# Optimization experiments

Measured on AMD Instinct MI355X. Metric: run time of the kernel, lower is better.

The kernel has to match this reference:

```python
import jax, jax.numpy as jnp
import numpy as np

N = 100_000   # nodes
E = 1_600_000 # edges (avg degree 16)
IN_DIM = 128
OUT_DIM = 64
NEG_SLOPE = 0.2  # PyG GATConv default


def setup_inputs() -> dict:
    key = jax.random.key(0)
    k_x, k_ei, k_w, k_as, k_ad = jax.random.split(key, 5)
    x = jax.random.normal(k_x, (N, IN_DIM), dtype=jnp.float32)
    edge_index = jax.random.randint(k_ei, (2, E), 0, N, dtype=jnp.int32)
    # GATConv params (heads=1): linear weight, attention vectors, output bias
    W = jax.random.normal(k_w, (IN_DIM, OUT_DIM), dtype=jnp.float32) / np.sqrt(IN_DIM)
    a_src = jax.random.normal(k_as, (OUT_DIM,), dtype=jnp.float32) * 0.1
    a_dst = jax.random.normal(k_ad, (OUT_DIM,), dtype=jnp.float32) * 0.1
    bias = jnp.zeros((OUT_DIM,), dtype=jnp.float32)
    return {"x": x, "edge_index": edge_index, "W": W, "a_src": a_src, "a_dst": a_dst, "bias": bias}


def reference(x, edge_index, W, a_src, a_dst, bias):
    # PyG GATConv, heads=1, add_self_loops=True
    h = x @ W                                   # [N, OUT]
    loop = jnp.arange(N, dtype=edge_index.dtype)
    ei = jnp.concatenate([edge_index, jnp.stack([loop, loop])], axis=1)  # [2, E+N]
    src, dst = ei[0], ei[1]
    # per-node attention logits, gathered per edge
    alpha_s = h @ a_src                         # [N]
    alpha_d = h @ a_dst                         # [N]
    e = alpha_s[src] + alpha_d[dst]             # [E+N]
    e = jnp.where(e > 0, e, NEG_SLOPE * e)      # leaky_relu
    # segment softmax over edges sharing the same destination node
    m = jax.ops.segment_max(e, dst, num_segments=N)   # every node has a self loop
    ex = jnp.exp(e - m[dst])
    s = jax.ops.segment_sum(ex, dst, num_segments=N)
    alpha = ex / s[dst]                         # [E+N]
    # weighted scatter-add of source messages
    out = jax.ops.segment_sum(alpha[:, None] * h[src], dst, num_segments=N)  # [N, OUT]
    return out + bias
```

## Files before the change

### kernel.cpp

```cpp
#include <hip/hip_runtime.h>
#include <hip/hip_bf16.h>

#ifndef NEG_SLOPE
#define NEG_SLOPE 0.2f
#endif

#define GRP_SHIFT 9
#define GRP_SIZE 512
#define NGMAX 256
#define MS_CHUNK 8192
#define BKT_CAP 10240

typedef short bf16x8 __attribute__((ext_vector_type(8)));
typedef float f32x4 __attribute__((ext_vector_type(4)));

__device__ __forceinline__ unsigned short f2bf(float f) {
    union { float f; unsigned int u; } c; c.f = f;
    unsigned int r = (c.u + 0x7FFFu + ((c.u >> 16) & 1u)) >> 16;
    return (unsigned short)r;
}
__device__ __forceinline__ float bf2f(unsigned short u) {
    union { unsigned int u; float f; } c; c.u = ((unsigned int)u) << 16;
    return c.f;
}
__device__ __forceinline__ float bflo(unsigned int u) {
    union { unsigned int u; float f; } c; c.u = u << 16;
    return c.f;
}
__device__ __forceinline__ float bfhi(unsigned int u) {
    union { unsigned int u; float f; } c; c.u = u & 0xffff0000u;
    return c.f;
}

__global__ __launch_bounds__(256) void gemm_kernel(
    const float* __restrict__ x, const float* __restrict__ W,
    const float* __restrict__ a_src, const float* __restrict__ a_dst,
    unsigned short* __restrict__ hb, float* __restrict__ as_,
    float* __restrict__ ad_, int* __restrict__ cursor, int N, int NG)
{
    __shared__ unsigned short xb[64 * 136];
    __shared__ unsigned short wt[64 * 136];

    const int tid = threadIdx.x;
    const int r0 = blockIdx.x * 64;

    if (blockIdx.x == 0) {
        for (int i = tid; i < NG; i += 256) cursor[i] = i * BKT_CAP;
    }

    for (int idx = tid; idx < 2048; idx += 256) {
        const int r = idx >> 5;
        const int c4 = idx & 31;
        const int row = r0 + r;
        float4 v = make_float4(0.f, 0.f, 0.f, 0.f);
        if (row < N) v = ((const float4*)(x + (size_t)row * 128))[c4];
        ushort4 o;
        o.x = f2bf(v.x); o.y = f2bf(v.y); o.z = f2bf(v.z); o.w = f2bf(v.w);
        *(ushort4*)(xb + r * 136 + c4 * 4) = o;
    }
    {
        const int n = tid & 63;
        const int kb = (tid >> 6) * 32;
        for (int kk = 0; kk < 32; ++kk) {
            const int k = kb + kk;
            wt[n * 136 + k] = f2bf(W[k * 64 + n]);
        }
    }
    __syncthreads();

    const int wv = tid >> 6;
    const int lane = tid & 63;
    const int m16 = lane & 15;
    const int quad = lane >> 4;

    f32x4 acc[4];
#pragma unroll
    for (int ct = 0; ct < 4; ++ct) acc[ct] = (f32x4){0.f, 0.f, 0.f, 0.f};

    const unsigned short* xrow = xb + (wv * 16 + m16) * 136;
#pragma unroll
    for (int kq = 0; kq < 4; ++kq) {
        const int k0 = kq * 32;
        const bf16x8 a = *(const bf16x8*)(xrow + k0 + quad * 8);
#pragma unroll
        for (int ct = 0; ct < 4; ++ct) {
            const bf16x8 b = *(const bf16x8*)(wt + (ct * 16 + m16) * 136 + k0 + quad * 8);
            acc[ct] = __builtin_amdgcn_mfma_f32_16x16x32_bf16(a, b, acc[ct], 0, 0, 0);
        }
    }

#pragma unroll
    for (int ct = 0; ct < 4; ++ct) {
#pragma unroll
        for (int rg = 0; rg < 4; ++rg) {
            const int row = r0 + wv * 16 + quad * 4 + rg;
            if (row < N) hb[(size_t)row * 64 + ct * 16 + m16] = f2bf(acc[ct][rg]);
        }
    }

    float asv[4], adv[4];
#pragma unroll
    for (int ct = 0; ct < 4; ++ct) {
        asv[ct] = a_src[ct * 16 + m16];
        adv[ct] = a_dst[ct * 16 + m16];
    }
#pragma unroll
    for (int rg = 0; rg < 4; ++rg) {
        float ps = acc[0][rg] * asv[0] + acc[1][rg] * asv[1] +
                   acc[2][rg] * asv[2] + acc[3][rg] * asv[3];
        float pd = acc[0][rg] * adv[0] + acc[1][rg] * adv[1] +
                   acc[2][rg] * adv[2] + acc[3][rg] * adv[3];
#pragma unroll
        for (int off = 1; off < 16; off <<= 1) {
            ps += __shfl_xor(ps, off);
            pd += __shfl_xor(pd, off);
        }
        const int row = r0 + wv * 16 + quad * 4 + rg;
        if (m16 == 0 && row < N) { as_[row] = ps; ad_[row] = pd; }
    }
}

__global__ __launch_bounds__(256) void multisplit_kernel(
    const int* __restrict__ ei, int* __restrict__ cursor,
    unsigned int* __restrict__ pairs, int E, int NG)
{
    __shared__ unsigned int ls_pack[MS_CHUNK];
    __shared__ unsigned char ls_g[MS_CHUNK];
    __shared__ int ls_hist[NGMAX];
    __shared__ int ls_gb[NGMAX];
    __shared__ int ls_wsum[4];

    const int tid = threadIdx.x;
    const int cs = blockIdx.x * MS_CHUNK;
    const int n = min(MS_CHUNK, E - cs);
    const int* srcp = ei + cs;
    const int* dstp = ei + E + cs;

    ls_hist[tid] = 0;
    __syncthreads();
    for (int i = tid; i < n; i += 256)
        atomicAdd(&ls_hist[dstp[i] >> GRP_SHIFT], 1);
    __syncthreads();

    const int h = ls_hist[tid];
    const int lane = tid & 63;
    int incl = h;
#pragma unroll
    for (int off = 1; off < 64; off <<= 1) {
        const int t = __shfl_up(incl, off);
        if (lane >= off) incl += t;
    }
    const int wv = tid >> 6;
    if (lane == 63) ls_wsum[wv] = incl;
    __syncthreads();
    int wpre = 0;
    for (int w = 0; w < wv; ++w) wpre += ls_wsum[w];
    const int excl = wpre + incl - h;
    if (tid < NG && h > 0) {
        const int gb = atomicAdd(&cursor[tid], h);
        ls_gb[tid] = gb - excl;
    }
    __syncthreads();
    ls_hist[tid] = excl;
    __syncthreads();

    for (int i = tid; i < n; i += 256) {
        const int src = srcp[i];
        const int dst = dstp[i];
        const int g = dst >> GRP_SHIFT;
        const int idx = atomicAdd(&ls_hist[g], 1);
        ls_pack[idx] = ((unsigned int)src << GRP_SHIFT) | (unsigned int)(dst & (GRP_SIZE - 1));
        ls_g[idx] = (unsigned char)g;
    }
    __syncthreads();

    for (int i = tid; i < n; i += 256) {
        const int g = ls_g[i];
        const int pos = ls_gb[g] + i;
        if (pos < (g + 1) * BKT_CAP)
            pairs[pos] = ls_pack[i];
    }
}

__global__ __launch_bounds__(256) void group_sort_kernel(
    const unsigned int* __restrict__ pairs, const int* __restrict__ cursor,
    unsigned int* __restrict__ meta, int* __restrict__ csr, int N)
{
    __shared__ int sdeg[GRP_SIZE];
    __shared__ int scur[GRP_SIZE];
    __shared__ int swsum[4];
    __shared__ int ssrc[BKT_CAP];
    const int g = blockIdx.x;
    const int tid = threadIdx.x;
    const int eb0 = g * BKT_CAP;
    const int cnt = min(cursor[g] - eb0, BKT_CAP);

    sdeg[tid] = 0;
    sdeg[tid + 256] = 0;
    __syncthreads();
    for (int i = tid; i < cnt; i += 256)
        atomicAdd(&sdeg[pairs[eb0 + i] & (GRP_SIZE - 1)], 1);
    __syncthreads();

    const int b0 = tid * 2;
    const int h0 = sdeg[b0], h1 = sdeg[b0 + 1];
    const int s = h0 + h1;
    const int lane = tid & 63;
    int incl = s;
#pragma unroll
    for (int off = 1; off < 64; off <<= 1) {
        const int t = __shfl_up(incl, off);
        if (lane >= off) incl += t;
    }
    const int wv = tid >> 6;
    if (lane == 63) swsum[wv] = incl;
    __syncthreads();
    int wpre = 0;
    for (int w = 0; w < wv; ++w) wpre += swsum[w];
    const int excl = wpre + incl - s;
    scur[b0] = excl;
    scur[b0 + 1] = excl + h0;
    {
        const int n0 = (g << GRP_SHIFT) + b0;
        if (n0 < N)
            meta[n0] = ((unsigned int)(eb0 + excl) << 10) | (unsigned int)min(h0, 1023);
        if (n0 + 1 < N)
            meta[n0 + 1] = ((unsigned int)(eb0 + excl + h0) << 10) | (unsigned int)min(h1, 1023);
    }
    __syncthreads();

    for (int i = tid; i < cnt; i += 256) {
        const unsigned int p = pairs[eb0 + i];
        const int idx = atomicAdd(&scur[p & (GRP_SIZE - 1)], 1);
        ssrc[idx] = (int)(p >> GRP_SHIFT);
    }
    __syncthreads();
    for (int i = tid; i < cnt; i += 256)
        csr[eb0 + i] = ssrc[i];
}

__global__ __launch_bounds__(256) void aggregate_kernel(
    const unsigned short* __restrict__ h, const float* __restrict__ as_,
    const float* __restrict__ ad_, const unsigned int* __restrict__ meta,
    const int* __restrict__ csr, const float* __restrict__ bias,
    float* __restrict__ out, int N)
{
    const int wid = (blockIdx.x * 256 + threadIdx.x) >> 6;
    const int lane = threadIdx.x & 63;
    if (wid >= N) return;

    const unsigned int mt = meta[wid];
    const int p0 = (int)(mt >> 10);
    const int deg = (int)(mt & 1023u);
    const float adi = ad_[wid];
    float e0 = as_[wid] + adi;
    e0 = e0 > 0.f ? e0 : NEG_SLOPE * e0;

    if (deg <= 63) {
        int s = wid;
        float e = -1e30f;
        if (lane < deg) {
            s = csr[p0 + lane];
            const float t = as_[s] + adi;
            e = t > 0.f ? t : NEG_SLOPE * t;
        } else if (lane == deg) {
            e = e0;
        }
        float m = e;
#pragma unroll
        for (int off = 1; off < 64; off <<= 1) m = fmaxf(m, __shfl_xor(m, off));
        const float pe = __expf(e - m);
        float l = pe;
#pragma unroll
        for (int off = 1; off < 64; off <<= 1) l += __shfl_xor(l, off);

        const int half = lane >> 5;
        const int l5 = lane & 31;
        const unsigned int* hb32 = (const unsigned int*)h;
        float acc0 = 0.f, acc1 = 0.f;
        const int npair = (deg + 2) >> 1;

        int jp = 0;
        for (; jp + 4 <= npair; jp += 4) {
            const int sl0 = (jp    ) * 2 + half;
            const int sl1 = (jp + 1) * 2 + half;
            const int sl2 = (jp + 2) * 2 + half;
            const int sl3 = (jp + 3) * 2 + half;
            const int s0 = __shfl(s, sl0), s1 = __shfl(s, sl1);
            const int s2 = __shfl(s, sl2), s3 = __shfl(s, sl3);
            const float w0 = __shfl(pe, sl0), w1 = __shfl(pe, sl1);
            const float w2 = __shfl(pe, sl2), w3 = __shfl(pe, sl3);
            const unsigned int u0 = hb32[s0 * 32 + l5];
            const unsigned int u1 = hb32[s1 * 32 + l5];
            const unsigned int u2 = hb32[s2 * 32 + l5];
            const unsigned int u3 = hb32[s3 * 32 + l5];
            acc0 += w0 * bflo(u0); acc1 += w0 * bfhi(u0);
            acc0 += w1 * bflo(u1); acc1 += w1 * bfhi(u1);
            acc0 += w2 * bflo(u2); acc1 += w2 * bfhi(u2);
            acc0 += w3 * bflo(u3); acc1 += w3 * bfhi(u3);
        }
        for (; jp < npair; ++jp) {
            const int sl = jp * 2 + half;
            const int sj = __shfl(s, sl);
            const float wj = __shfl(pe, sl);
            const unsigned int u = hb32[sj * 32 + l5];
            acc0 += wj * bflo(u);
            acc1 += wj * bfhi(u);
        }
        acc0 += __shfl_xor(acc0, 32);
        acc1 += __shfl_xor(acc1, 32);
        if (half == 0) {
            const float2 bv = ((const float2*)bias)[l5];
            float2 o;
            o.x = acc0 / l + bv.x;
            o.y = acc1 / l + bv.y;
            ((float2*)(out + (size_t)wid * 64))[l5] = o;
        }
    } else {
        float m = e0, ll = 1.f;
        float acc = bf2f(h[(size_t)wid * 64 + lane]);
        const int p1 = p0 + deg;
        for (int p = p0; p < p1; ++p) {
            const int sj = csr[p];
            float ee = as_[sj] + adi;
            ee = ee > 0.f ? ee : NEG_SLOPE * ee;
            const float nm = fmaxf(m, ee);
            const float sc = __expf(m - nm);
            const float pp = __expf(ee - nm);
            ll = ll * sc + pp;
            acc = acc * sc + pp * bf2f(h[(size_t)sj * 64 + lane]);
            m = nm;
        }
        out[(size_t)wid * 64 + lane] = acc / ll + bias[lane];
    }
}

extern "C" void kernel_launch(void* const* d_in, const int* in_sizes, int n_in,
                              void* d_out, int out_size, void* d_ws, size_t ws_size,
                              hipStream_t stream)
{
    const float* x     = (const float*)d_in[0];
    const int*   ei    = (const int*)d_in[1];
    const float* W     = (const float*)d_in[2];
    const float* a_src = (const float*)d_in[3];
    const float* a_dst = (const float*)d_in[4];
    const float* bias  = (const float*)d_in[5];
    float* out = (float*)d_out;

    const int N = in_sizes[0] / 128;
    const int E = in_sizes[1] / 2;
    const int NG = (N + GRP_SIZE - 1) >> GRP_SHIFT;
    const int nchunk = (E + MS_CHUNK - 1) / MS_CHUNK;

    unsigned short* hb = (unsigned short*)d_ws;
    float* alpha_s = (float*)(hb + (size_t)N * 64);
    float* alpha_d = alpha_s + N;
    int* cursor = (int*)(alpha_d + N);
    unsigned int* meta = (unsigned int*)(cursor + NG);
    int* csr = (int*)(meta + N);
    unsigned int* pairs = (unsigned int*)(csr + (size_t)NG * BKT_CAP);

    gemm_kernel<<<(N + 63) / 64, 256, 0, stream>>>(x, W, a_src, a_dst, hb,
                                                   alpha_s, alpha_d, cursor, N, NG);
    multisplit_kernel<<<nchunk, 256, 0, stream>>>(ei, cursor, pairs, E, NG);
    group_sort_kernel<<<NG, 256, 0, stream>>>(pairs, cursor, meta, csr, N);
    aggregate_kernel<<<(N + 3) / 4, 256, 0, stream>>>(hb, alpha_s, alpha_d, meta,
                                                      csr, bias, out, N);
}
```

Baseline: 215.0 us.

## Fuse GEMM with edge multisplit, widen group sort, process two nodes per wave

The GEMM and the edge multisplit now run as one launch with branch-selected block roles and a shared-memory union, and the cursor is zeroed by a memset so the two independent stages can overlap. The group sort runs with 1024 threads per block, one thread per destination slot. Aggregation assigns two destination nodes to each wave and interleaves their gathers to raise memory-level parallelism. In exchange, the fused kernel's shared-memory footprint follows the larger multisplit layout, and the paired loop does wasted shuffles and gathers when the two degrees differ.

```diff
diff --git a/kernel.cpp b/kernel.cpp
--- a/kernel.cpp
+++ b/kernel.cpp
@@ -32,211 +32,246 @@
     return c.f;
 }
 
-__global__ __launch_bounds__(256) void gemm_kernel(
+struct GemmSmem {
+    unsigned short xb[64 * 136];
+    unsigned short wt[64 * 136];
+};
+struct MsSmem {
+    unsigned int pack[MS_CHUNK];
+    unsigned char gtag[MS_CHUNK];
+    int hist[NGMAX];
+    int gb[NGMAX];
+    int wsum[4];
+};
+union FusedSmem {
+    GemmSmem g;
+    MsSmem m;
+};
+
+__global__ __launch_bounds__(256) void gemm_ms_kernel(
     const float* __restrict__ x, const float* __restrict__ W,
     const float* __restrict__ a_src, const float* __restrict__ a_dst,
     unsigned short* __restrict__ hb, float* __restrict__ as_,
-    float* __restrict__ ad_, int* __restrict__ cursor, int N, int NG)
+    float* __restrict__ ad_, const int* __restrict__ ei,
+    int* __restrict__ cursor, unsigned int* __restrict__ pairs,
+    int N, int E, int NG, int gemmBlocks)
 {
-    __shared__ unsigned short xb[64 * 136];
-    __shared__ unsigned short wt[64 * 136];
-
+    __shared__ FusedSmem sm;
     const int tid = threadIdx.x;
-    const int r0 = blockIdx.x * 64;
-
-    if (blockIdx.x == 0) {
-        for (int i = tid; i < NG; i += 256) cursor[i] = i * BKT_CAP;
-    }
-
-    for (int idx = tid; idx < 2048; idx += 256) {
-        const int r = idx >> 5;
-        const int c4 = idx & 31;
-        const int row = r0 + r;
-        float4 v = make_float4(0.f, 0.f, 0.f, 0.f);
-        if (row < N) v = ((const float4*)(x + (size_t)row * 128))[c4];
-        ushort4 o;
-        o.x = f2bf(v.x); o.y = f2bf(v.y); o.z = f2bf(v.z); o.w = f2bf(v.w);
-        *(ushort4*)(xb + r * 136 + c4 * 4) = o;
-    }
-    {
-        const int n = tid & 63;
-        const int kb = (tid >> 6) * 32;
-        for (int kk = 0; kk < 32; ++kk) {
-            const int k = kb + kk;
-            wt[n * 136 + k] = f2bf(W[k * 64 + n]);
-        }
-    }
-    __syncthreads();
-
-    const int wv = tid >> 6;
-    const int lane = tid & 63;
-    const int m16 = lane & 15;
-    const int quad = lane >> 4;
-
-    f32x4 acc[4];
-#pragma unroll
-    for (int ct = 0; ct < 4; ++ct) acc[ct] = (f32x4){0.f, 0.f, 0.f, 0.f};
-
-    const unsigned short* xrow = xb + (wv * 16 + m16) * 136;
-#pragma unroll
-    for (int kq = 0; kq < 4; ++kq) {
-        const int k0 = kq * 32;
-        const bf16x8 a = *(const bf16x8*)(xrow + k0 + quad * 8);
+
+    if ((int)blockIdx.x < gemmBlocks) {
+        unsigned short* xb = sm.g.xb;
+        unsigned short* wt = sm.g.wt;
+        const int r0 = blockIdx.x * 64;
+
+        for (int idx = tid; idx < 2048; idx += 256) {
+            const int r = idx >> 5;
+            const int c4 = idx & 31;
+            const int row = r0 + r;
+            float4 v = make_float4(0.f, 0.f, 0.f, 0.f);
+            if (row < N) v = ((const float4*)(x + (size_t)row * 128))[c4];
+            ushort4 o;
+            o.x = f2bf(v.x); o.y = f2bf(v.y); o.z = f2bf(v.z); o.w = f2bf(v.w);
+            *(ushort4*)(xb + r * 136 + c4 * 4) = o;
+        }
+        {
+            const int n = tid & 63;
+            const int kb = (tid >> 6) * 32;
+            for (int kk = 0; kk < 32; ++kk) {
+                const int k = kb + kk;
+                wt[n * 136 + k] = f2bf(W[k * 64 + n]);
+            }
+        }
+        __syncthreads();
+
+        const int wv = tid >> 6;
+        const int lane = tid & 63;
+        const int m16 = lane & 15;
+        const int quad = lane >> 4;
+
+        f32x4 acc[4];
+#pragma unroll
+        for (int ct = 0; ct < 4; ++ct) acc[ct] = (f32x4){0.f, 0.f, 0.f, 0.f};
+
+        const unsigned short* xrow = xb + (wv * 16 + m16) * 136;
+#pragma unroll
+        for (int kq = 0; kq < 4; ++kq) {
+            const int k0 = kq * 32;
+            const bf16x8 a = *(const bf16x8*)(xrow + k0 + quad * 8);
+#pragma unroll
+            for (int ct = 0; ct < 4; ++ct) {
+                const bf16x8 b = *(const bf16x8*)(wt + (ct * 16 + m16) * 136 + k0 + quad * 8);
+                acc[ct] = __builtin_amdgcn_mfma_f32_16x16x32_bf16(a, b, acc[ct], 0, 0, 0);
+            }
+        }
+
 #pragma unroll
         for (int ct = 0; ct < 4; ++ct) {
-            const bf16x8 b = *(const bf16x8*)(wt + (ct * 16 + m16) * 136 + k0 + quad * 8);
-            acc[ct] = __builtin_amdgcn_mfma_f32_16x16x32_bf16(a, b, acc[ct], 0, 0, 0);
-        }
-    }
-
-#pragma unroll
-    for (int ct = 0; ct < 4; ++ct) {
+#pragma unroll
+            for (int rg = 0; rg < 4; ++rg) {
+                const int row = r0 + wv * 16 + quad * 4 + rg;
+                if (row < N) hb[(size_t)row * 64 + ct * 16 + m16] = f2bf(acc[ct][rg]);
+            }
+        }
+
+        float asv[4], adv[4];
+#pragma unroll
+        for (int ct = 0; ct < 4; ++ct) {
+            asv[ct] = a_src[ct * 16 + m16];
+            adv[ct] = a_dst[ct * 16 + m16];
+        }
 #pragma unroll
         for (int rg = 0; rg < 4; ++rg) {
+            float ps = acc[0][rg] * asv[0] + acc[1][rg] * asv[1] +
+                       acc[2][rg] * asv[2] + acc[3][rg] * asv[3];
+            float pd = acc[0][rg] * adv[0] + acc[1][rg] * adv[1] +
+                       acc[2][rg] * adv[2] + acc[3][rg] * adv[3];
+#pragma unroll
+            for (int off = 1; off < 16; off <<= 1) {
+                ps += __shfl_xor(ps, off);
+                pd += __shfl_xor(pd, off);
+            }
             const int row = r0 + wv * 16 + quad * 4 + rg;
-            if (row < N) hb[(size_t)row * 64 + ct * 16 + m16] = f2bf(acc[ct][rg]);
-        }
-    }
-
-    float asv[4], adv[4];
-#pragma unroll
-    for (int ct = 0; ct < 4; ++ct) {
-        asv[ct] = a_src[ct * 16 + m16];
-        adv[ct] = a_dst[ct * 16 + m16];
-    }
-#pragma unroll
-    for (int rg = 0; rg < 4; ++rg) {
-        float ps = acc[0][rg] * asv[0] + acc[1][rg] * asv[1] +
-                   acc[2][rg] * asv[2] + acc[3][rg] * asv[3];
-        float pd = acc[0][rg] * adv[0] + acc[1][rg] * adv[1] +
-                   acc[2][rg] * adv[2] + acc[3][rg] * adv[3];
-#pragma unroll
-        for (int off = 1; off < 16; off <<= 1) {
-            ps += __shfl_xor(ps, off);
-            pd += __shfl_xor(pd, off);
-        }
-        const int row = r0 + wv * 16 + quad * 4 + rg;
-        if (m16 == 0 && row < N) { as_[row] = ps; ad_[row] = pd; }
-    }
-}
-
-__global__ __launch_bounds__(256) void multisplit_kernel(
-    const int* __restrict__ ei, int* __restrict__ cursor,
-    unsigned int* __restrict__ pairs, int E, int NG)
-{
-    __shared__ unsigned int ls_pack[MS_CHUNK];
-    __shared__ unsigned char ls_g[MS_CHUNK];
-    __shared__ int ls_hist[NGMAX];
-    __shared__ int ls_gb[NGMAX];
-    __shared__ int ls_wsum[4];
-
-    const int tid = threadIdx.x;
-    const int cs = blockIdx.x * MS_CHUNK;
-    const int n = min(MS_CHUNK, E - cs);
-    const int* srcp = ei + cs;
-    const int* dstp = ei + E + cs;
-
-    ls_hist[tid] = 0;
-    __syncthreads();
-    for (int i = tid; i < n; i += 256)
-        atomicAdd(&ls_hist[dstp[i] >> GRP_SHIFT], 1);
-    __syncthreads();
-
-    const int h = ls_hist[tid];
-    const int lane = tid & 63;
-    int incl = h;
-#pragma unroll
-    for (int off = 1; off < 64; off <<= 1) {
-        const int t = __shfl_up(incl, off);
-        if (lane >= off) incl += t;
-    }
-    const int wv = tid >> 6;
-    if (lane == 63) ls_wsum[wv] = incl;
-    __syncthreads();
-    int wpre = 0;
-    for (int w = 0; w < wv; ++w) wpre += ls_wsum[w];
-    const int excl = wpre + incl - h;
-    if (tid < NG && h > 0) {
-        const int gb = atomicAdd(&cursor[tid], h);
-        ls_gb[tid] = gb - excl;
-    }
-    __syncthreads();
-    ls_hist[tid] = excl;
-    __syncthreads();
-
-    for (int i = tid; i < n; i += 256) {
-        const int src = srcp[i];
-        const int dst = dstp[i];
-        const int g = dst >> GRP_SHIFT;
-        const int idx = atomicAdd(&ls_hist[g], 1);
-        ls_pack[idx] = ((unsigned int)src << GRP_SHIFT) | (unsigned int)(dst & (GRP_SIZE - 1));
-        ls_g[idx] = (unsigned char)g;
-    }
-    __syncthreads();
-
-    for (int i = tid; i < n; i += 256) {
-        const int g = ls_g[i];
-        const int pos = ls_gb[g] + i;
-        if (pos < (g + 1) * BKT_CAP)
-            pairs[pos] = ls_pack[i];
-    }
-}
-
-__global__ __launch_bounds__(256) void group_sort_kernel(
+            if (m16 == 0 && row < N) { as_[row] = ps; ad_[row] = pd; }
+        }
+    } else {
+        unsigned int* ls_pack = sm.m.pack;
+        unsigned char* ls_g = sm.m.gtag;
+        int* ls_hist = sm.m.hist;
+        int* ls_gb = sm.m.gb;
+        int* ls_wsum = sm.m.wsum;
+
+        const int cid = (int)blockIdx.x - gemmBlocks;
+        const int cs = cid * MS_CHUNK;
+        const int n = min(MS_CHUNK, E - cs);
+        const int* srcp = ei + cs;
+        const int* dstp = ei + E + cs;
+
+        ls_hist[tid] = 0;
+        __syncthreads();
+        for (int i = tid; i < n; i += 256)
+            atomicAdd(&ls_hist[dstp[i] >> GRP_SHIFT], 1);
+        __syncthreads();
+
+        const int h = ls_hist[tid];
+        const int lane = tid & 63;
+        int incl = h;
+#pragma unroll
+        for (int off = 1; off < 64; off <<= 1) {
+            const int t = __shfl_up(incl, off);
+            if (lane >= off) incl += t;
+        }
+        const int wv = tid >> 6;
+        if (lane == 63) ls_wsum[wv] = incl;
+        __syncthreads();
+        int wpre = 0;
+        for (int w = 0; w < wv; ++w) wpre += ls_wsum[w];
+        const int excl = wpre + incl - h;
+        if (tid < NG && h > 0) {
+            const int old = atomicAdd(&cursor[tid], h);
+            ls_gb[tid] = tid * BKT_CAP + old - excl;
+        }
+        __syncthreads();
+        ls_hist[tid] = excl;
+        __syncthreads();
+
+        for (int i = tid; i < n; i += 256) {
+            const int src = srcp[i];
+            const int dst = dstp[i];
+            const int g = dst >> GRP_SHIFT;
+            const int idx = atomicAdd(&ls_hist[g], 1);
+            ls_pack[idx] = ((unsigned int)src << GRP_SHIFT) | (unsigned int)(dst & (GRP_SIZE - 1));
+            ls_g[idx] = (unsigned char)g;
+        }
+        __syncthreads();
+
+        for (int i = tid; i < n; i += 256) {
+            const int g = ls_g[i];
+            const int pos = ls_gb[g] + i;
+            if (pos < (g + 1) * BKT_CAP)
+                pairs[pos] = ls_pack[i];
+        }
+    }
+}
+
+__global__ __launch_bounds__(1024) void group_sort_kernel(
     const unsigned int* __restrict__ pairs, const int* __restrict__ cursor,
     unsigned int* __restrict__ meta, int* __restrict__ csr, int N)
 {
     __shared__ int sdeg[GRP_SIZE];
     __shared__ int scur[GRP_SIZE];
-    __shared__ int swsum[4];
+    __shared__ int swsum[8];
     __shared__ int ssrc[BKT_CAP];
     const int g = blockIdx.x;
     const int tid = threadIdx.x;
     const int eb0 = g * BKT_CAP;
-    const int cnt = min(cursor[g] - eb0, BKT_CAP);
-
-    sdeg[tid] = 0;
-    sdeg[tid + 256] = 0;
+    const int cnt = min(cursor[g], BKT_CAP);
+
+    if (tid < GRP_SIZE) sdeg[tid] = 0;
     __syncthreads();
-    for (int i = tid; i < cnt; i += 256)
+    for (int i = tid; i < cnt; i += 1024)
         atomicAdd(&sdeg[pairs[eb0 + i] & (GRP_SIZE - 1)], 1);
     __syncthreads();
 
-    const int b0 = tid * 2;
-    const int h0 = sdeg[b0], h1 = sdeg[b0 + 1];
-    const int s = h0 + h1;
-    const int lane = tid & 63;
-    int incl = s;
-#pragma unroll
-    for (int off = 1; off < 64; off <<= 1) {
-        const int t = __shfl_up(incl, off);
-        if (lane >= off) incl += t;
-    }
-    const int wv = tid >> 6;
-    if (lane == 63) swsum[wv] = incl;
+    int s = 0, incl = 0;
+    if (tid < GRP_SIZE) {
+        s = sdeg[tid];
+        const int lane = tid & 63;
+        incl = s;
+#pragma unroll
+        for (int off = 1; off < 64; off <<= 1) {
+            const int t = __shfl_up(incl, off);
+            if (lane >= off) incl += t;
+        }
+        if (lane == 63) swsum[tid >> 6] = incl;
+    }
     __syncthreads();
-    int wpre = 0;
-    for (int w = 0; w < wv; ++w) wpre += swsum[w];
-    const int excl = wpre + incl - s;
-    scur[b0] = excl;
-    scur[b0 + 1] = excl + h0;
-    {
-        const int n0 = (g << GRP_SHIFT) + b0;
-        if (n0 < N)
-            meta[n0] = ((unsigned int)(eb0 + excl) << 10) | (unsigned int)min(h0, 1023);
-        if (n0 + 1 < N)
-            meta[n0 + 1] = ((unsigned int)(eb0 + excl + h0) << 10) | (unsigned int)min(h1, 1023);
+    if (tid < GRP_SIZE) {
+        int wpre = 0;
+        const int wv = tid >> 6;
+        for (int w = 0; w < wv; ++w) wpre += swsum[w];
+        const int excl = wpre + incl - s;
+        scur[tid] = excl;
+        const int node = (g << GRP_SHIFT) + tid;
+        if (node < N)
+            meta[node] = ((unsigned int)(eb0 + excl) << 10) | (unsigned int)min(s, 1023);
     }
     __syncthreads();
 
-    for (int i = tid; i < cnt; i += 256) {
+    for (int i = tid; i < cnt; i += 1024) {
         const unsigned int p = pairs[eb0 + i];
         const int idx = atomicAdd(&scur[p & (GRP_SIZE - 1)], 1);
         ssrc[idx] = (int)(p >> GRP_SHIFT);
     }
     __syncthreads();
-    for (int i = tid; i < cnt; i += 256)
+    for (int i = tid; i < cnt; i += 1024)
         csr[eb0 + i] = ssrc[i];
+}
+
+__device__ void aggregate_slow(
+    const unsigned short* __restrict__ h, const float* __restrict__ as_,
+    const float* __restrict__ ad_, const int* __restrict__ csr,
+    const float* __restrict__ bias, float* __restrict__ out,
+    int wid, int p0, int deg, int lane)
+{
+    const float adi = ad_[wid];
+    float e0 = as_[wid] + adi;
+    e0 = e0 > 0.f ? e0 : NEG_SLOPE * e0;
+    float m = e0, ll = 1.f;
+    float acc = bf2f(h[(size_t)wid * 64 + lane]);
+    const int p1 = p0 + deg;
+    for (int p = p0; p < p1; ++p) {
+        const int sj = csr[p];
+        float ee = as_[sj] + adi;
+        ee = ee > 0.f ? ee : NEG_SLOPE * ee;
+        const float nm = fmaxf(m, ee);
+        const float sc = __expf(m - nm);
+        const float pp = __expf(ee - nm);
+        ll = ll * sc + pp;
+        acc = acc * sc + pp * bf2f(h[(size_t)sj * 64 + lane]);
+        m = nm;
+    }
+    out[(size_t)wid * 64 + lane] = acc / ll + bias[lane];
 }
 
 __global__ __launch_bounds__(256) void aggregate_kernel(
@@ -245,93 +280,118 @@
     const int* __restrict__ csr, const float* __restrict__ bias,
     float* __restrict__ out, int N)
 {
-    const int wid = (blockIdx.x * 256 + threadIdx.x) >> 6;
+    const int wbase = (blockIdx.x * 256 + threadIdx.x) >> 6;
     const int lane = threadIdx.x & 63;
-    if (wid >= N) return;
-
-    const unsigned int mt = meta[wid];
-    const int p0 = (int)(mt >> 10);
-    const int deg = (int)(mt & 1023u);
-    const float adi = ad_[wid];
-    float e0 = as_[wid] + adi;
-    e0 = e0 > 0.f ? e0 : NEG_SLOPE * e0;
-
-    if (deg <= 63) {
-        int s = wid;
-        float e = -1e30f;
-        if (lane < deg) {
-            s = csr[p0 + lane];
-            const float t = as_[s] + adi;
-            e = t > 0.f ? t : NEG_SLOPE * t;
-        } else if (lane == deg) {
-            e = e0;
-        }
-        float m = e;
-#pragma unroll
-        for (int off = 1; off < 64; off <<= 1) m = fmaxf(m, __shfl_xor(m, off));
-        const float pe = __expf(e - m);
-        float l = pe;
-#pragma unroll
-        for (int off = 1; off < 64; off <<= 1) l += __shfl_xor(l, off);
+    const int widA = wbase * 2;
+    if (widA >= N) return;
+    const int widB = widA + 1;
+    const bool hasB = (widB < N);
+
+    const unsigned int mtA = meta[widA];
+    const unsigned int mtB = hasB ? meta[widB] : 0u;
+    const int p0A = (int)(mtA >> 10), degA = (int)(mtA & 1023u);
+    const int p0B = (int)(mtB >> 10), degB = (int)(mtB & 1023u);
+
+    if (degA <= 63 && degB <= 63) {
+        const float adiA = ad_[widA];
+        const float adiB = hasB ? ad_[widB] : 0.f;
+        float e0A = as_[widA] + adiA;
+        e0A = e0A > 0.f ? e0A : NEG_SLOPE * e0A;
+        float e0B = hasB ? as_[widB] + adiB : 0.f;
+        e0B = e0B > 0.f ? e0B : NEG_SLOPE * e0B;
+
+        int sA = widA, sB = hasB ? widB : widA;
+        float eA = -1e30f, eB = -1e30f;
+        if (lane < degA) {
+            sA = csr[p0A + lane];
+            const float t = as_[sA] + adiA;
+            eA = t > 0.f ? t : NEG_SLOPE * t;
+        } else if (lane == degA) {
+            eA = e0A;
+        }
+        if (hasB) {
+            if (lane < degB) {
+                sB = csr[p0B + lane];
+                const float t = as_[sB] + adiB;
+                eB = t > 0.f ? t : NEG_SLOPE * t;
+            } else if (lane == degB) {
+                eB = e0B;
+            }
+        }
+
+        float mA = eA, mB = eB;
+#pragma unroll
+        for (int off = 1; off < 64; off <<= 1) {
+            mA = fmaxf(mA, __shfl_xor(mA, off));
+            mB = fmaxf(mB, __shfl_xor(mB, off));
+        }
+        const float peA = __expf(eA - mA);
+        const float peB = hasB ? __expf(eB - mB) : 0.f;
+        float lA = peA, lB = peB;
+#pragma unroll
+        for (int off = 1; off < 64; off <<= 1) {
+            lA += __shfl_xor(lA, off);
+            lB += __shfl_xor(lB, off);
+        }
 
         const int half = lane >> 5;
         const int l5 = lane & 31;
         const unsigned int* hb32 = (const unsigned int*)h;
-        float acc0 = 0.f, acc1 = 0.f;
-        const int npair = (deg + 2) >> 1;
-
-        int jp = 0;
-        for (; jp + 4 <= npair; jp += 4) {
+        float a0 = 0.f, a1 = 0.f, b0 = 0.f, b1 = 0.f;
+        const int npA = (degA + 2) >> 1;
+        const int npB = hasB ? (degB + 2) >> 1 : 0;
+        const int npMax = max(npA, npB);
+
+        for (int jp = 0; jp < npMax; jp += 4) {
             const int sl0 = (jp    ) * 2 + half;
             const int sl1 = (jp + 1) * 2 + half;
             const int sl2 = (jp + 2) * 2 + half;
             const int sl3 = (jp + 3) * 2 + half;
-            const int s0 = __shfl(s, sl0), s1 = __shfl(s, sl1);
-            const int s2 = __shfl(s, sl2), s3 = __shfl(s, sl3);
-            const float w0 = __shfl(pe, sl0), w1 = __shfl(pe, sl1);
-            const float w2 = __shfl(pe, sl2), w3 = __shfl(pe, sl3);
-            const unsigned int u0 = hb32[s0 * 32 + l5];
-            const unsigned int u1 = hb32[s1 * 32 + l5];
-            const unsigned int u2 = hb32[s2 * 32 + l5];
-            const unsigned int u3 = hb32[s3 * 32 + l5];
-            acc0 += w0 * bflo(u0); acc1 += w0 * bfhi(u0);
-            acc0 += w1 * bflo(u1); acc1 += w1 * bfhi(u1);
-            acc0 += w2 * bflo(u2); acc1 += w2 * bfhi(u2);
-            acc0 += w3 * bflo(u3); acc1 += w3 * bfhi(u3);
-        }
-        for (; jp < npair; ++jp) {
-            const int sl = jp * 2 + half;
-            const int sj = __shfl(s, sl);
-            const float wj = __shfl(pe, sl);
-            const unsigned int u = hb32[sj * 32 + l5];
-            acc0 += wj * bflo(u);
-            acc1 += wj * bfhi(u);
-        }
-        acc0 += __shfl_xor(acc0, 32);
-        acc1 += __shfl_xor(acc1, 32);
+            const int sa0 = __shfl(sA, sl0), sa1 = __shfl(sA, sl1);
+            const int sa2 = __shfl(sA, sl2), sa3 = __shfl(sA, sl3);
+            const int sb0 = __shfl(sB, sl0), sb1 = __shfl(sB, sl1);
+            const int sb2 = __shfl(sB, sl2), sb3 = __shfl(sB, sl3);
+            const float wa0 = __shfl(peA, sl0), wa1 = __shfl(peA, sl1);
+            const float wa2 = __shfl(peA, sl2), wa3 = __shfl(peA, sl3);
+            const float wb0 = __shfl(peB, sl0), wb1 = __shfl(peB, sl1);
+            const float wb2 = __shfl(peB, sl2), wb3 = __shfl(peB, sl3);
+            const unsigned int ua0 = hb32[sa0 * 32 + l5];
+            const unsigned int ua1 = hb32[sa1 * 32 + l5];
+            const unsigned int ua2 = hb32[sa2 * 32 + l5];
+            const unsigned int ua3 = hb32[sa3 * 32 + l5];
+            const unsigned int ub0 = hb32[sb0 * 32 + l5];
+            const unsigned int ub1 = hb32[sb1 * 32 + l5];
+            const unsigned int ub2 = hb32[sb2 * 32 + l5];
+            const unsigned int ub3 = hb32[sb3 * 32 + l5];
+            a0 += wa0 * bflo(ua0); a1 += wa0 * bfhi(ua0);
+            a0 += wa1 * bflo(ua1); a1 += wa1 * bfhi(ua1);
+            a0 += wa2 * bflo(ua2); a1 += wa2 * bfhi(ua2);
+            a0 += wa3 * bflo(ua3); a1 += wa3 * bfhi(ua3);
+            b0 += wb0 * bflo(ub0); b1 += wb0 * bfhi(ub0);
+            b0 += wb1 * bflo(ub1); b1 += wb1 * bfhi(ub1);
+            b0 += wb2 * bflo(ub2); b1 += wb2 * bfhi(ub2);
+            b0 += wb3 * bflo(ub3); b1 += wb3 * bfhi(ub3);
+        }
+        a0 += __shfl_xor(a0, 32);
+        a1 += __shfl_xor(a1, 32);
+        b0 += __shfl_xor(b0, 32);
+        b1 += __shfl_xor(b1, 32);
         if (half == 0) {
             const float2 bv = ((const float2*)bias)[l5];
-            float2 o;
-            o.x = acc0 / l + bv.x;
-            o.y = acc1 / l + bv.y;
-            ((float2*)(out + (size_t)wid * 64))[l5] = o;
+            float2 oA;
+            oA.x = a0 / lA + bv.x;
+            oA.y = a1 / lA + bv.y;
+            ((float2*)(out + (size_t)widA * 64))[l5] = oA;
+            if (hasB) {
+                float2 oB;
+                oB.x = b0 / lB + bv.x;
+                oB.y = b1 / lB + bv.y;
+                ((float2*)(out + (size_t)widB * 64))[l5] = oB;
+            }
         }
     } else {
-        float m = e0, ll = 1.f;
-        float acc = bf2f(h[(size_t)wid * 64 + lane]);
-        const int p1 = p0 + deg;
-        for (int p = p0; p < p1; ++p) {
-            const int sj = csr[p];
-            float ee = as_[sj] + adi;
-            ee = ee > 0.f ? ee : NEG_SLOPE * ee;
-            const float nm = fmaxf(m, ee);
-            const float sc = __expf(m - nm);
-            const float pp = __expf(ee - nm);
-            ll = ll * sc + pp;
-            acc = acc * sc + pp * bf2f(h[(size_t)sj * 64 + lane]);
-            m = nm;
-        }
-        out[(size_t)wid * 64 + lane] = acc / ll + bias[lane];
+        aggregate_slow(h, as_, ad_, csr, bias, out, widA, p0A, degA, lane);
+        if (hasB) aggregate_slow(h, as_, ad_, csr, bias, out, widB, p0B, degB, lane);
     }
 }
 
@@ -351,6 +411,7 @@
     const int E = in_sizes[1] / 2;
     const int NG = (N + GRP_SIZE - 1) >> GRP_SHIFT;
     const int nchunk = (E + MS_CHUNK - 1) / MS_CHUNK;
+    const int gemmBlocks = (N + 63) / 64;
 
     unsigned short* hb = (unsigned short*)d_ws;
     float* alpha_s = (float*)(hb + (size_t)N * 64);
@@ -360,10 +421,11 @@
     int* csr = (int*)(meta + N);
     unsigned int* pairs = (unsigned int*)(csr + (size_t)NG * BKT_CAP);
 
-    gemm_kernel<<<(N + 63) / 64, 256, 0, stream>>>(x, W, a_src, a_dst, hb,
-                                                   alpha_s, alpha_d, cursor, N, NG);
-    multisplit_kernel<<<nchunk, 256, 0, stream>>>(ei, cursor, pairs, E, NG);
-    group_sort_kernel<<<NG, 256, 0, stream>>>(pairs, cursor, meta, csr, N);
-    aggregate_kernel<<<(N + 3) / 4, 256, 0, stream>>>(hb, alpha_s, alpha_d, meta,
+    hipMemsetAsync(cursor, 0, (size_t)NG * sizeof(int), stream);
+    gemm_ms_kernel<<<gemmBlocks + nchunk, 256, 0, stream>>>(
+        x, W, a_src, a_dst, hb, alpha_s, alpha_d, ei, cursor, pairs,
+        N, E, NG, gemmBlocks);
+    group_sort_kernel<<<NG, 1024, 0, stream>>>(pairs, cursor, meta, csr, N);
+    aggregate_kernel<<<(N + 7) / 8, 256, 0, stream>>>(hb, alpha_s, alpha_d, meta,
                                                       csr, bias, out, N);
 }
```

Result: faster. 191.7 us (-10.9%).
